# Kernel optimization log

Measured on AMD Instinct MI355X. Metric: run time of the kernel, lower is better.

Reference implementation:

```python
import jax, jax.numpy as jnp
import numpy as np

EPS = 1e-5

def setup_inputs() -> dict:
    key = jax.random.key(0)
    ks = jax.random.split(key, 4)
    B, N, L, D, H = 1, 32, 512, 256, 8
    msa = jax.random.normal(ks[0], (B, N, L, D), dtype=jnp.float32)
    pair_bias = jax.random.normal(ks[1], (B, L, L, H), dtype=jnp.float32)
    # parameters (fan-in scaled like nn.Linear init magnitude)
    w_qkv = jax.random.normal(ks[2], (D, 3 * D), dtype=jnp.float32) / np.sqrt(D)
    b_qkv = jnp.zeros((3 * D,), dtype=jnp.float32)
    w_proj = jax.random.normal(ks[3], (D, D), dtype=jnp.float32) / np.sqrt(D)
    b_proj = jnp.zeros((D,), dtype=jnp.float32)
    ln_w = jnp.ones((D,), dtype=jnp.float32)
    ln_b = jnp.zeros((D,), dtype=jnp.float32)
    return {"msa": msa, "pair_bias": pair_bias, "ln_w": ln_w, "ln_b": ln_b,
            "w_qkv": w_qkv, "b_qkv": b_qkv, "w_proj": w_proj, "b_proj": b_proj}

def reference(msa, pair_bias, ln_w, ln_b, w_qkv, b_qkv, w_proj, b_proj):
    B, N, L, D = msa.shape
    H = pair_bias.shape[-1]
    hd = D // H
    # LayerNorm over last dim (biased variance, eps=1e-5, as in nn.LayerNorm)
    mu = jnp.mean(msa, axis=-1, keepdims=True)
    var = jnp.mean(jnp.square(msa - mu), axis=-1, keepdims=True)
    m = (msa - mu) * jax.lax.rsqrt(var + EPS) * ln_w + ln_b
    # fused QKV projection; output dim 3*D splits as (3, H, hd)
    qkv = jnp.einsum('bnld,de->bnle', m, w_qkv) + b_qkv  # (B,N,L,3D)
    qkv = qkv.reshape(B, N, L, 3, H, hd)
    q = qkv[:, :, :, 0]  # (B,N,L,H,hd)
    k = qkv[:, :, :, 1]
    v = qkv[:, :, :, 2]
    scale = 1.0 / np.sqrt(hd).astype(np.float32)
    attn = jnp.einsum('bnqhd,bnkhd->bnhqk', q, k) * scale  # (B,N,H,L,L)
    # pair bias (B,L,L,H) -> (B,1,H,L,L), broadcast over the N_seq rows
    attn = attn + jnp.transpose(pair_bias, (0, 3, 1, 2))[:, None]
    attn = jax.nn.softmax(attn, axis=-1)
    out = jnp.einsum('bnhqk,bnkhd->bnqhd', attn, v).reshape(B, N, L, D)
    out = jnp.einsum('bnld,de->bnle', out, w_proj) + b_proj
    return msa + out
```

## Files before the change

### kernel.cpp

```cpp
#include <hip/hip_runtime.h>
#include <hip/hip_bf16.h>

typedef __attribute__((ext_vector_type(8))) short short8;
typedef __attribute__((ext_vector_type(4))) float f32x4;

#define LOG2E 1.4426950408889634f
#define QSCALE 0.25505403955318165f

static __device__ __forceinline__ unsigned short f2bf(float f){
  union { float f; unsigned u; } v; v.f = f;
  unsigned r = v.u + 0x7fffu + ((v.u >> 16) & 1u);
  return (unsigned short)(r >> 16);
}
static __device__ __forceinline__ float bf2f(unsigned short s){
  union { unsigned u; float f; } v; v.u = ((unsigned)s) << 16; return v.f;
}
static __device__ __forceinline__ unsigned cvt_pk_bf16(float lo, float hi){
  unsigned r;
  asm("v_cvt_pk_bf16_f32 %0, %1, %2" : "=v"(r) : "v"(lo), "v"(hi));
  return r;
}
static __device__ __forceinline__ void gload_lds16(const void* g, void* l){
  __builtin_amdgcn_global_load_lds((const __attribute__((address_space(1))) unsigned*)g,
                                   (__attribute__((address_space(3))) unsigned*)l, 16, 0, 0);
}

__global__ __launch_bounds__(256) void k_prep(
    const float* __restrict__ w_qkv, const float* __restrict__ w_proj,
    const float* __restrict__ pb, const float* __restrict__ msa,
    const float* __restrict__ ln_w, const float* __restrict__ ln_b,
    unsigned short* __restrict__ wqkvT, unsigned short* __restrict__ wprojT,
    unsigned short* __restrict__ bt, unsigned short* __restrict__ m_bf){
  __shared__ float tile[64][65];
  int b = blockIdx.x;
  int tid = threadIdx.x;
  if (b < 64){
    const float* in;
    unsigned short* outp;
    int C, tc;
    if (b < 48){ in = w_qkv; outp = wqkvT; C = 768; tc = 12; b -= 0; }
    else       { in = w_proj; outp = wprojT; C = 256; tc = 4;  b -= 48; }
    int r0 = (b / tc) * 64, c0 = (b % tc) * 64;
#pragma unroll
    for (int it = 0; it < 16; it++){
      int idx = tid + it*256, ri = idx >> 6, ci = idx & 63;
      tile[ri][ci] = in[(size_t)(r0+ri)*C + c0+ci];
    }
    __syncthreads();
#pragma unroll
    for (int it = 0; it < 16; it++){
      int idx = tid + it*256, co = idx >> 6, ro = idx & 63;
      outp[(size_t)(c0+co)*256 + r0+ro] = f2bf(tile[ro][co]);
    }
  } else if (b < 1088){
    int bid = b - 64;
    int q = bid >> 1;
    int k = ((bid & 1) << 8) + tid;
    int kc = k >> 6, tl = (k >> 4) & 3, gg = (k >> 2) & 3, r = k & 3;
    int kp = kc*64 + gg*16 + tl*4 + r;
    const float* src = pb + ((size_t)q * 512 + k) * 8;
    float4 a = *(const float4*)src;
    float4 c = *(const float4*)(src + 4);
    float hv[8] = {a.x, a.y, a.z, a.w, c.x, c.y, c.z, c.w};
#pragma unroll
    for (int hh = 0; hh < 8; hh++)
      bt[((size_t)hh * 512 + q) * 512 + kp] = f2bf(hv[hh] * LOG2E);
  } else {
    int wave = tid >> 6, lane = tid & 63;
    int row = (b - 1088) * 4 + wave;
    const float* xr = msa + (size_t)row * 256 + lane * 4;
    float4 v = *(const float4*)xr;
    float s  = v.x + v.y + v.z + v.w;
    float sq = v.x*v.x + v.y*v.y + v.z*v.z + v.w*v.w;
#pragma unroll
    for (int off = 1; off < 64; off <<= 1){ s += __shfl_xor(s, off); sq += __shfl_xor(sq, off); }
    float mu = s * (1.0f/256.0f);
    float var = sq * (1.0f/256.0f) - mu*mu;
    float rs = rsqrtf(var + 1e-5f);
    float4 wv = *(const float4*)(ln_w + lane*4);
    float4 bv = *(const float4*)(ln_b + lane*4);
    uint2 o;
    o.x = cvt_pk_bf16((v.x-mu)*rs*wv.x + bv.x, (v.y-mu)*rs*wv.y + bv.y);
    o.y = cvt_pk_bf16((v.z-mu)*rs*wv.z + bv.z, (v.w-mu)*rs*wv.w + bv.w);
    *(uint2*)(m_bf + (size_t)row * 256 + lane * 4) = o;
  }
}

__global__ __launch_bounds__(256) void k_gemm_qkv(const unsigned short* __restrict__ A,
    const unsigned short* __restrict__ Bt, const float* __restrict__ bias,
    unsigned short* __restrict__ Qb, unsigned short* __restrict__ Kb, unsigned short* __restrict__ Vb){
  __shared__ unsigned short As[128*64];
  __shared__ unsigned short Bs[128*64];
  int bid = blockIdx.x;
  int bn = bid % 6, bm = bid / 6;
  int m0 = bm * 128, e0 = bn * 128;
  int t = threadIdx.x, lane = t & 63, w = t >> 6;
  int wm = w >> 1, wn = w & 1;
  int g = lane >> 4, mm = lane & 15;
  f32x4 acc[4][4] = {};
  for (int k0 = 0; k0 < 256; k0 += 64){
    __syncthreads();
#pragma unroll
    for (int it = 0; it < 4; it++){
      int task = t + it * 256;
      int row = task >> 3, ch = task & 7;
      gload_lds16(A  + (size_t)(m0+row)*256 + k0 + ch*8, &As[task*8]);
      gload_lds16(Bt + (size_t)(e0+row)*256 + k0 + ch*8, &Bs[task*8]);
    }
    __syncthreads();
#pragma unroll
    for (int kst = 0; kst < 2; kst++){
      short8 a[4], bb[4];
#pragma unroll
      for (int i = 0; i < 4; i++)
        a[i]  = *(short8*)(&As[(wm*64 + i*16 + mm)*64 + kst*32 + g*8]);
#pragma unroll
      for (int j = 0; j < 4; j++)
        bb[j] = *(short8*)(&Bs[(wn*64 + j*16 + mm)*64 + kst*32 + g*8]);
#pragma unroll
      for (int i = 0; i < 4; i++)
#pragma unroll
        for (int j = 0; j < 4; j++)
          acc[i][j] = __builtin_amdgcn_mfma_f32_16x16x32_bf16(a[i], bb[j], acc[i][j], 0, 0, 0);
    }
  }
#pragma unroll
  for (int i = 0; i < 4; i++)
#pragma unroll
    for (int j = 0; j < 4; j++){
      int col = e0 + wn*64 + j*16 + mm;
      float bc = bias[col];
      int sidx = col >> 8, hh = (col >> 5) & 7, d = col & 31;
      unsigned short* dst = (sidx == 0) ? Qb : ((sidx == 1) ? Kb : Vb);
      float sc = (sidx == 0) ? QSCALE : 1.0f;
#pragma unroll
      for (int r = 0; r < 4; r++){
        int gm = m0 + wm*64 + i*16 + 4*g + r;
        int nn = gm >> 9, l = gm & 511;
        dst[(((size_t)nn*8 + hh)*512 + l)*32 + d] = f2bf((acc[i][j][r] + bc) * sc);
      }
    }
}

__global__ __launch_bounds__(512) void k_attn(const unsigned short* __restrict__ Qb,
    const unsigned short* __restrict__ Kb, const unsigned short* __restrict__ Vb,
    const unsigned short* __restrict__ bt, unsigned short* __restrict__ Ob){
  __shared__ unsigned short Ks[512*40];
  __shared__ unsigned short Vs[32*520];
  int bid = blockIdx.x;
  int h = bid & 7;
  int n = (bid >> 3) & 31;
  int qq = bid >> 8;
  int nh = n*8 + h;
  int t = threadIdx.x;
  int lane = t & 63, wv = t >> 6;
  int g = lane >> 4, q16 = lane & 15;
  const unsigned short* kbase = Kb + (size_t)nh * 16384;
  const unsigned short* vbase = Vb + (size_t)nh * 16384;
  const unsigned short* qbase = Qb + (size_t)nh * 16384;
  {
    int row = t;
    const uint4* ksrc = (const uint4*)(kbase + row * 32);
#pragma unroll
    for (int j = 0; j < 4; j++) *(uint4*)(&Ks[row*40 + j*8]) = ksrc[j];
    int prow = (row & ~12) | ((row & 4) << 1) | ((row & 8) >> 1);
    const uint* vsrc = (const uint*)(vbase + row * 32);
    uint vv[16];
#pragma unroll
    for (int j = 0; j < 16; j++) vv[j] = vsrc[j];
#pragma unroll
    for (int j = 0; j < 16; j++){
      Vs[(2*j)*520 + prow]   = (unsigned short)(vv[j] & 0xffffu);
      Vs[(2*j+1)*520 + prow] = (unsigned short)(vv[j] >> 16);
    }
  }
  __syncthreads();
  {
    int qb = qq*128 + wv*16;
    int qg = qb + q16;
    short8 qf = *(const short8*)(qbase + (size_t)qg * 32 + g * 8);
    const unsigned short* bq = bt + ((size_t)(h*512 + qg))*512 + g*16;
    f32x4 ls4 = {0.0f, 0.0f, 0.0f, 0.0f};
    f32x4 acc[2] = {{0,0,0,0},{0,0,0,0}};
    f32x4 zf = {0.0f, 0.0f, 0.0f, 0.0f};
    uint4 bn0 = *(const uint4*)(bq);
    uint4 bn1 = *(const uint4*)(bq + 8);
#pragma unroll 2
    for (int kc = 0; kc < 8; kc++){
      union { uint4 w[2]; unsigned short u[16]; } bu;
      bu.w[0] = bn0; bu.w[1] = bn1;
      if (kc < 7){
        bn0 = *(const uint4*)(bq + (kc+1)*64);
        bn1 = *(const uint4*)(bq + (kc+1)*64 + 8);
      }
      f32x4 s[4];
      __builtin_amdgcn_s_setprio(1);
#pragma unroll
      for (int tl = 0; tl < 4; tl++){
        short8 kf = *(short8*)(&Ks[(kc*64 + tl*16 + q16)*40 + g*8]);
        s[tl] = __builtin_amdgcn_mfma_f32_16x16x32_bf16(kf, qf, zf, 0, 0, 0);
      }
      __builtin_amdgcn_s_setprio(0);
#pragma unroll
      for (int tl = 0; tl < 4; tl++){
        f32x4 pz;
#pragma unroll
        for (int r = 0; r < 4; r++){
          float e = __builtin_amdgcn_exp2f(s[tl][r] + bf2f(bu.u[tl*4+r]));
          pz[r] = e;
          ls4[r] += e;
        }
        s[tl] = pz;
      }
#pragma unroll
      for (int cl = 0; cl < 2; cl++){
        unsigned a0 = cvt_pk_bf16(s[2*cl][0],   s[2*cl][1]);
        unsigned a1 = cvt_pk_bf16(s[2*cl][2],   s[2*cl][3]);
        unsigned b0 = cvt_pk_bf16(s[2*cl+1][0], s[2*cl+1][1]);
        unsigned b1 = cvt_pk_bf16(s[2*cl+1][2], s[2*cl+1][3]);
        asm("v_permlane32_swap_b32 %0, %1" : "+v"(a0), "+v"(b0));
        asm("v_permlane32_swap_b32 %0, %1" : "+v"(a1), "+v"(b1));
        union { unsigned w[4]; short8 pf; } u;
        u.w[0] = a0; u.w[1] = a1; u.w[2] = b0; u.w[3] = b1;
        __builtin_amdgcn_s_setprio(1);
#pragma unroll
        for (int half = 0; half < 2; half++){
          short8 vf = *(short8*)(&Vs[(half*16 + q16)*520 + kc*64 + cl*32 + g*8]);
          acc[half] = __builtin_amdgcn_mfma_f32_16x16x32_bf16(u.pf, vf, acc[half], 0, 0, 0);
        }
        __builtin_amdgcn_s_setprio(0);
      }
    }
    float ls = (ls4[0] + ls4[1]) + (ls4[2] + ls4[3]);
    ls += __shfl_xor(ls, 16);
    ls += __shfl_xor(ls, 32);
    float linv[4];
#pragma unroll
    for (int r = 0; r < 4; r++) linv[r] = 1.0f / __shfl(ls, 4*g + r);
#pragma unroll
    for (int half = 0; half < 2; half++)
#pragma unroll
      for (int r = 0; r < 4; r++){
        int ql = qb + 4*g + r;
        Ob[((size_t)n*512 + ql)*256 + h*32 + half*16 + q16] = f2bf(acc[half][r] * linv[r]);
      }
  }
}

__global__ __launch_bounds__(256) void k_gemm_proj(const unsigned short* __restrict__ A,
    const unsigned short* __restrict__ Bt, const float* __restrict__ bias,
    const float* __restrict__ msa, float* __restrict__ out){
  __shared__ unsigned short As[64*64];
  __shared__ unsigned short Bs[128*64];
  int bid = blockIdx.x;
  int bn = bid & 1, bm = bid >> 1;
  int m0 = bm * 64, e0 = bn * 128;
  int t = threadIdx.x, lane = t & 63, w = t >> 6;
  int g = lane >> 4, mm = lane & 15;
  f32x4 acc[4][2] = {};
  for (int k0 = 0; k0 < 256; k0 += 64){
    __syncthreads();
#pragma unroll
    for (int it = 0; it < 2; it++){
      int task = t + it * 256;
      gload_lds16(A + (size_t)(m0+(task>>3))*256 + k0 + (task&7)*8, &As[task*8]);
    }
#pragma unroll
    for (int it = 0; it < 4; it++){
      int task = t + it * 256;
      gload_lds16(Bt + (size_t)(e0+(task>>3))*256 + k0 + (task&7)*8, &Bs[task*8]);
    }
    __syncthreads();
#pragma unroll
    for (int kst = 0; kst < 2; kst++){
      short8 a[4], bb[2];
#pragma unroll
      for (int i = 0; i < 4; i++)
        a[i] = *(short8*)(&As[(i*16 + mm)*64 + kst*32 + g*8]);
#pragma unroll
      for (int j = 0; j < 2; j++)
        bb[j] = *(short8*)(&Bs[(w*32 + j*16 + mm)*64 + kst*32 + g*8]);
#pragma unroll
      for (int i = 0; i < 4; i++)
#pragma unroll
        for (int j = 0; j < 2; j++)
          acc[i][j] = __builtin_amdgcn_mfma_f32_16x16x32_bf16(a[i], bb[j], acc[i][j], 0, 0, 0);
    }
  }
#pragma unroll
  for (int i = 0; i < 4; i++)
#pragma unroll
    for (int j = 0; j < 2; j++){
      int col = e0 + w*32 + j*16 + mm;
      float bc = bias[col];
#pragma unroll
      for (int r = 0; r < 4; r++){
        int gm = m0 + i*16 + 4*g + r;
        size_t idx = (size_t)gm * 256 + col;
        out[idx] = acc[i][j][r] + bc + msa[idx];
      }
    }
}

extern "C" void kernel_launch(void* const* d_in, const int* in_sizes, int n_in,
                              void* d_out, int out_size, void* d_ws, size_t ws_size,
                              hipStream_t stream){
  const float* msa    = (const float*)d_in[0];
  const float* pb     = (const float*)d_in[1];
  const float* ln_w   = (const float*)d_in[2];
  const float* ln_b   = (const float*)d_in[3];
  const float* w_qkv  = (const float*)d_in[4];
  const float* b_qkv  = (const float*)d_in[5];
  const float* w_proj = (const float*)d_in[6];
  const float* b_proj = (const float*)d_in[7];

  unsigned short* ws     = (unsigned short*)d_ws;
  unsigned short* m_bf   = ws;
  unsigned short* wqkvT  = m_bf   + 4194304;
  unsigned short* wprojT = wqkvT  + 196608;
  unsigned short* Qb     = wprojT + 65536;
  unsigned short* Kb     = Qb     + 4194304;
  unsigned short* Vb     = Kb     + 4194304;
  unsigned short* Ob     = Vb     + 4194304;
  unsigned short* bt     = Ob     + 4194304;
  float* out = (float*)d_out;

  k_prep<<<5184, 256, 0, stream>>>(w_qkv, w_proj, pb, msa, ln_w, ln_b, wqkvT, wprojT, bt, m_bf);
  k_gemm_qkv<<<768, 256, 0, stream>>>(m_bf, wqkvT, b_qkv, Qb, Kb, Vb);
  k_attn<<<1024, 512, 0, stream>>>(Qb, Kb, Vb, bt, Ob);
  k_gemm_proj<<<512, 256, 0, stream>>>(Ob, wprojT, b_proj, msa, out);
}
```

Baseline: 67.97 us.

## Fold pair bias into MFMA accumulator and compute softmax row sums via MFMA

The attention kernel now loads the pair bias as fp32 and passes it as the MFMA C operand, so the bias add happens inside the QK^T instruction instead of as a separate VALU add. Softmax row sums are produced by an extra MFMA against a ones vector, which replaces per-lane accumulation and the cross-lane shuffle reduction. The bias transpose moves out of the prep kernel into its own kernel, launched after the QKV GEMM, and writes fp32 into the now-free m_bf buffer. This doubles the bias traffic read by attention and adds a kernel launch plus one MFMA per chunk. Row sums are also now taken from bf16-rounded probabilities.

Measured after the change: 86.34 us. 27.0% more time.

```diff
diff --git a/kernel.cpp b/kernel.cpp
--- a/kernel.cpp
+++ b/kernel.cpp
@@ -12,9 +12,6 @@
   unsigned r = v.u + 0x7fffu + ((v.u >> 16) & 1u);
   return (unsigned short)(r >> 16);
 }
-static __device__ __forceinline__ float bf2f(unsigned short s){
-  union { unsigned u; float f; } v; v.u = ((unsigned)s) << 16; return v.f;
-}
 static __device__ __forceinline__ unsigned cvt_pk_bf16(float lo, float hi){
   unsigned r;
   asm("v_cvt_pk_bf16_f32 %0, %1, %2" : "=v"(r) : "v"(lo), "v"(hi));
@@ -27,10 +24,10 @@
 
 __global__ __launch_bounds__(256) void k_prep(
     const float* __restrict__ w_qkv, const float* __restrict__ w_proj,
-    const float* __restrict__ pb, const float* __restrict__ msa,
+    const float* __restrict__ msa,
     const float* __restrict__ ln_w, const float* __restrict__ ln_b,
     unsigned short* __restrict__ wqkvT, unsigned short* __restrict__ wprojT,
-    unsigned short* __restrict__ bt, unsigned short* __restrict__ m_bf){
+    unsigned short* __restrict__ m_bf){
   __shared__ float tile[64][65];
   int b = blockIdx.x;
   int tid = threadIdx.x;
@@ -52,22 +49,9 @@
       int idx = tid + it*256, co = idx >> 6, ro = idx & 63;
       outp[(size_t)(c0+co)*256 + r0+ro] = f2bf(tile[ro][co]);
     }
-  } else if (b < 1088){
-    int bid = b - 64;
-    int q = bid >> 1;
-    int k = ((bid & 1) << 8) + tid;
-    int kc = k >> 6, tl = (k >> 4) & 3, gg = (k >> 2) & 3, r = k & 3;
-    int kp = kc*64 + gg*16 + tl*4 + r;
-    const float* src = pb + ((size_t)q * 512 + k) * 8;
-    float4 a = *(const float4*)src;
-    float4 c = *(const float4*)(src + 4);
-    float hv[8] = {a.x, a.y, a.z, a.w, c.x, c.y, c.z, c.w};
-#pragma unroll
-    for (int hh = 0; hh < 8; hh++)
-      bt[((size_t)hh * 512 + q) * 512 + kp] = f2bf(hv[hh] * LOG2E);
   } else {
     int wave = tid >> 6, lane = tid & 63;
-    int row = (b - 1088) * 4 + wave;
+    int row = (b - 64) * 4 + wave;
     const float* xr = msa + (size_t)row * 256 + lane * 4;
     float4 v = *(const float4*)xr;
     float s  = v.x + v.y + v.z + v.w;
@@ -84,6 +68,21 @@
     o.y = cvt_pk_bf16((v.z-mu)*rs*wv.z + bv.z, (v.w-mu)*rs*wv.w + bv.w);
     *(uint2*)(m_bf + (size_t)row * 256 + lane * 4) = o;
   }
+}
+
+__global__ void k_bias_t(const float* __restrict__ pb, float* __restrict__ btf){
+  int bid = blockIdx.x;
+  int q = bid >> 1;
+  int k = ((bid & 1) << 8) + threadIdx.x;
+  int kc = k >> 6, tl = (k >> 4) & 3, gg = (k >> 2) & 3, r = k & 3;
+  int kp = kc*64 + gg*16 + tl*4 + r;
+  const float* src = pb + ((size_t)q * 512 + k) * 8;
+  float4 a = *(const float4*)src;
+  float4 c = *(const float4*)(src + 4);
+  float hv[8] = {a.x, a.y, a.z, a.w, c.x, c.y, c.z, c.w};
+#pragma unroll
+  for (int hh = 0; hh < 8; hh++)
+    btf[((size_t)hh * 512 + q) * 512 + kp] = hv[hh] * LOG2E;
 }
 
 __global__ __launch_bounds__(256) void k_gemm_qkv(const unsigned short* __restrict__ A,
@@ -144,7 +143,7 @@
 
 __global__ __launch_bounds__(512) void k_attn(const unsigned short* __restrict__ Qb,
     const unsigned short* __restrict__ Kb, const unsigned short* __restrict__ Vb,
-    const unsigned short* __restrict__ bt, unsigned short* __restrict__ Ob){
+    const float* __restrict__ btf, unsigned short* __restrict__ Ob){
   __shared__ unsigned short Ks[512*40];
   __shared__ unsigned short Vs[32*520];
   int bid = blockIdx.x;
@@ -179,39 +178,35 @@
     int qb = qq*128 + wv*16;
     int qg = qb + q16;
     short8 qf = *(const short8*)(qbase + (size_t)qg * 32 + g * 8);
-    const unsigned short* bq = bt + ((size_t)(h*512 + qg))*512 + g*16;
-    f32x4 ls4 = {0.0f, 0.0f, 0.0f, 0.0f};
+    const float* bq = btf + ((size_t)(h*512 + qg))*512 + g*16;
     f32x4 acc[2] = {{0,0,0,0},{0,0,0,0}};
-    f32x4 zf = {0.0f, 0.0f, 0.0f, 0.0f};
-    uint4 bn0 = *(const uint4*)(bq);
-    uint4 bn1 = *(const uint4*)(bq + 8);
+    f32x4 lsacc = {0.0f, 0.0f, 0.0f, 0.0f};
+    const short8 ones = {0x3F80,0x3F80,0x3F80,0x3F80,0x3F80,0x3F80,0x3F80,0x3F80};
+    f32x4 Cn[4];
+#pragma unroll
+    for (int j = 0; j < 4; j++) Cn[j] = *(const f32x4*)(bq + j*4);
 #pragma unroll 2
     for (int kc = 0; kc < 8; kc++){
-      union { uint4 w[2]; unsigned short u[16]; } bu;
-      bu.w[0] = bn0; bu.w[1] = bn1;
+      f32x4 Cc[4];
+#pragma unroll
+      for (int j = 0; j < 4; j++) Cc[j] = Cn[j];
       if (kc < 7){
-        bn0 = *(const uint4*)(bq + (kc+1)*64);
-        bn1 = *(const uint4*)(bq + (kc+1)*64 + 8);
+#pragma unroll
+        for (int j = 0; j < 4; j++) Cn[j] = *(const f32x4*)(bq + (kc+1)*64 + j*4);
       }
       f32x4 s[4];
       __builtin_amdgcn_s_setprio(1);
 #pragma unroll
       for (int tl = 0; tl < 4; tl++){
         short8 kf = *(short8*)(&Ks[(kc*64 + tl*16 + q16)*40 + g*8]);
-        s[tl] = __builtin_amdgcn_mfma_f32_16x16x32_bf16(kf, qf, zf, 0, 0, 0);
+        s[tl] = __builtin_amdgcn_mfma_f32_16x16x32_bf16(kf, qf, Cc[tl], 0, 0, 0);
       }
       __builtin_amdgcn_s_setprio(0);
 #pragma unroll
-      for (int tl = 0; tl < 4; tl++){
-        f32x4 pz;
-#pragma unroll
-        for (int r = 0; r < 4; r++){
-          float e = __builtin_amdgcn_exp2f(s[tl][r] + bf2f(bu.u[tl*4+r]));
-          pz[r] = e;
-          ls4[r] += e;
-        }
-        s[tl] = pz;
-      }
+      for (int tl = 0; tl < 4; tl++)
+#pragma unroll
+        for (int r = 0; r < 4; r++)
+          s[tl][r] = __builtin_amdgcn_exp2f(s[tl][r]);
 #pragma unroll
       for (int cl = 0; cl < 2; cl++){
         unsigned a0 = cvt_pk_bf16(s[2*cl][0],   s[2*cl][1]);
@@ -223,6 +218,7 @@
         union { unsigned w[4]; short8 pf; } u;
         u.w[0] = a0; u.w[1] = a1; u.w[2] = b0; u.w[3] = b1;
         __builtin_amdgcn_s_setprio(1);
+        lsacc = __builtin_amdgcn_mfma_f32_16x16x32_bf16(u.pf, ones, lsacc, 0, 0, 0);
 #pragma unroll
         for (int half = 0; half < 2; half++){
           short8 vf = *(short8*)(&Vs[(half*16 + q16)*520 + kc*64 + cl*32 + g*8]);
@@ -231,12 +227,9 @@
         __builtin_amdgcn_s_setprio(0);
       }
     }
-    float ls = (ls4[0] + ls4[1]) + (ls4[2] + ls4[3]);
-    ls += __shfl_xor(ls, 16);
-    ls += __shfl_xor(ls, 32);
     float linv[4];
 #pragma unroll
-    for (int r = 0; r < 4; r++) linv[r] = 1.0f / __shfl(ls, 4*g + r);
+    for (int r = 0; r < 4; r++) linv[r] = 1.0f / lsacc[r];
 #pragma unroll
     for (int half = 0; half < 2; half++)
 #pragma unroll
@@ -322,11 +315,12 @@
   unsigned short* Kb     = Qb     + 4194304;
   unsigned short* Vb     = Kb     + 4194304;
   unsigned short* Ob     = Vb     + 4194304;
-  unsigned short* bt     = Ob     + 4194304;
+  float* btf = (float*)m_bf;
   float* out = (float*)d_out;
 
-  k_prep<<<5184, 256, 0, stream>>>(w_qkv, w_proj, pb, msa, ln_w, ln_b, wqkvT, wprojT, bt, m_bf);
+  k_prep<<<4160, 256, 0, stream>>>(w_qkv, w_proj, msa, ln_w, ln_b, wqkvT, wprojT, m_bf);
   k_gemm_qkv<<<768, 256, 0, stream>>>(m_bf, wqkvT, b_qkv, Qb, Kb, Vb);
-  k_attn<<<1024, 512, 0, stream>>>(Qb, Kb, Vb, bt, Ob);
+  k_bias_t<<<1024, 256, 0, stream>>>(pb, btf);
+  k_attn<<<1024, 512, 0, stream>>>(Qb, Kb, Vb, btf, Ob);
   k_gemm_proj<<<512, 256, 0, stream>>>(Ob, wprojT, b_proj, msa, out);
 }
```
